# Kernel optimization log

Measured on AMD Instinct MI355X. Metric: run time of the kernel, lower is better.

Reference implementation:

```python
import jax, jax.numpy as jnp
import numpy as np

SEP = 64  # separate_number


def _get_histogram(M, sep):
    # torch code detaches + moves to CPU: no gradient flows through the histogram
    M = jax.lax.stop_gradient(M)
    mn = jnp.min(M)
    mx = jnp.max(M)
    interval = (mx - mn) / sep
    # equal-width binning; last bin is inclusive of max (clip handles it)
    idx = jnp.clip(jnp.floor((M - mn) / interval).astype(jnp.int32), 0, sep - 1)
    hist = jnp.zeros((sep,), dtype=M.dtype).at[idx.ravel()].add(1.0)
    return jax.nn.sigmoid(hist)


def setup_inputs() -> dict:
    key = jax.random.key(0)
    k1, k2, k3 = jax.random.split(key, 3)
    N, D = 8192, 256
    current_feature = jax.random.normal(k1, (N, D), dtype=jnp.float32)
    previous_feature = jax.random.normal(k2, (N, D), dtype=jnp.float32)
    # nn.Linear(separate_number, hidden_dim=1, bias=False) weight: [1, SEP]
    W = jax.random.normal(k3, (1, SEP), dtype=jnp.float32) * (1.0 / np.sqrt(SEP))
    return {"current_feature": current_feature, "previous_feature": previous_feature, "W": W}


def reference(current_feature, previous_feature, W):
    sep = W.shape[1]
    # [N, N] similarity matrix
    M = jnp.matmul(current_feature, previous_feature.T)
    hist_left = _get_histogram(M, sep)
    # result_matrix_right = prev @ cur.T = M.T; a transpose has an identical
    # value histogram, so reuse M (same math, avoids a second NxN matmul)
    hist_right = _get_histogram(M, sep)
    beta = (hist_left + hist_right) / 2.0
    beta = jnp.matmul(beta, W.T)  # Linear, no bias -> [hidden_dim]
    return jax.nn.sigmoid(beta)
```

## Files before the change

### kernel.cpp

```cpp
#include <hip/hip_runtime.h>

typedef __attribute__((ext_vector_type(8))) short short8v;
typedef __attribute__((ext_vector_type(4))) float f32x4;

#define N_ROWS 8192
#define KSPLIT 768
#define SEP 64
#define TDET 65.0f
#define TEXACT 73.0f
#define VTOL 5.5f
#define LIST_CAP 524288u

__device__ inline unsigned f2ord(float x){
  unsigned u = __float_as_uint(x);
  return (u & 0x80000000u) ? ~u : (u | 0x80000000u);
}
__device__ inline float ord2f(unsigned u){
  unsigned b = (u & 0x80000000u) ? (u & 0x7fffffffu) : ~u;
  return __uint_as_float(b);
}
__device__ inline unsigned short bf16rn(float x){
  unsigned b = __float_as_uint(x);
  unsigned r = (b + 0x7fffu + ((b >> 16) & 1u)) >> 16;
  return (unsigned short)r;
}
__device__ inline void gload16(const void* g, void* l){
  __builtin_amdgcn_global_load_lds((const __attribute__((address_space(1))) void*)g,
                                   (__attribute__((address_space(3))) void*)l, 16, 0, 0);
}
__device__ inline int bin_of(float v, float mnv, float interval){
  float r = (v - mnv) / interval;
  int b = (int)floorf(r);
  return b < 0 ? 0 : (b > 63 ? 63 : b);
}

__global__ void split_kernel(const float* __restrict__ cur, const float* __restrict__ prev,
                             unsigned short* __restrict__ cur2, unsigned short* __restrict__ prev2,
                             unsigned* __restrict__ ctl){
  if (blockIdx.x == 0){
    if (threadIdx.x == 0){
      ctl[0] = 0xFFFFFFFFu; ctl[1] = 0u; ctl[2] = 1u; ctl[3] = 0u; ctl[4] = 0u;
    }
    if (threadIdx.x < 64) ctl[5 + threadIdx.x] = 0u;
  }
  int g = blockIdx.x * blockDim.x + threadIdx.x;
  int isB = (g >= (N_ROWS * 256 / 4)) ? 1 : 0;
  int t = g - isB * (N_ROWS * 256 / 4);
  const float4 v = ((const float4*)(isB ? prev : cur))[t];
  int row = t >> 6;
  int col = (t & 63) << 2;
  float xs[4] = {v.x, v.y, v.z, v.w};
  unsigned short h[4], l[4];
  #pragma unroll
  for (int j = 0; j < 4; ++j){
    unsigned short hb = bf16rn(xs[j]);
    float hf = __uint_as_float(((unsigned)hb) << 16);
    h[j] = hb;
    l[j] = bf16rn(xs[j] - hf);
  }
  unsigned short* dst = isB ? prev2 : cur2;
  size_t base = (size_t)row * KSPLIT + col;
  uint2 hw, lw;
  hw.x = (unsigned)h[0] | ((unsigned)h[1] << 16); hw.y = (unsigned)h[2] | ((unsigned)h[3] << 16);
  lw.x = (unsigned)l[0] | ((unsigned)l[1] << 16); lw.y = (unsigned)l[2] | ((unsigned)l[3] << 16);
  *(uint2*)(dst + base) = hw;
  if (!isB){
    *(uint2*)(dst + base + 256) = lw;
    *(uint2*)(dst + base + 512) = hw;
  } else {
    *(uint2*)(dst + base + 256) = hw;
    *(uint2*)(dst + base + 512) = lw;
  }
}

__global__ __launch_bounds__(256) void gemm_det(const unsigned short* __restrict__ A2,
                                                const unsigned short* __restrict__ B2,
                                                unsigned* __restrict__ idxq,
                                                unsigned* __restrict__ lcnt){
  __shared__ unsigned short Ab[2][128 * 32];
  __shared__ unsigned short Bb[2][256 * 32];

  const int tid  = threadIdx.x;
  const int lane = tid & 63;
  const int wave = tid >> 6;
  const int swz = ((blockIdx.x & 7) << 8) | (blockIdx.x >> 3);
  const int bm = swz >> 5;
  const int bn = swz & 31;
  const int wr = wave >> 1, wc = wave & 1;

  const size_t aBase = (size_t)bm * 128 * KSPLIT;
  const size_t bBase = (size_t)bn * 256 * KSPLIT;
  const int rsel = lane & 15;
  const int ksel = (lane >> 4) * 8;

  f32x4 acc[4][8];
  #pragma unroll
  for (int m = 0; m < 4; ++m)
    #pragma unroll
    for (int n = 0; n < 8; ++n)
      acc[m][n] = (f32x4){0.f, 0.f, 0.f, 0.f};

  auto STAGE = [&](int ks, int b){
    const int k0 = ks * 32;
    #pragma unroll
    for (int r = 0; r < 2; ++r){
      int id = tid + r * 256;
      gload16(A2 + aBase + (size_t)(id >> 2) * KSPLIT + (id & 3) * 8 + k0, &Ab[b][id * 8]);
    }
    #pragma unroll
    for (int r = 0; r < 4; ++r){
      int id = tid + r * 256;
      gload16(B2 + bBase + (size_t)(id >> 2) * KSPLIT + (id & 3) * 8 + k0, &Bb[b][id * 8]);
    }
  };
  auto COMPUTE = [&](int b){
    short8v a[4];
    #pragma unroll
    for (int m = 0; m < 4; ++m)
      a[m] = *(const short8v*)(&Ab[b][(wr * 64 + m * 16 + rsel) * 32 + ksel]);
    #pragma unroll
    for (int n = 0; n < 8; ++n){
      short8v bv = *(const short8v*)(&Bb[b][(wc * 128 + n * 16 + rsel) * 32 + ksel]);
      #pragma unroll
      for (int m = 0; m < 4; ++m)
        acc[m][n] = __builtin_amdgcn_mfma_f32_16x16x32_bf16(a[m], bv, acc[m][n], 0, 0, 0);
    }
  };

  STAGE(0, 0);
  __syncthreads();
  for (int ks = 0; ks < 8; ++ks){
    if (ks < 7) STAGE(ks + 1, (ks + 1) & 1);
    COMPUTE(ks & 1);
    __syncthreads();
  }

  #pragma unroll
  for (int h2 = 0; h2 < 2; ++h2){
    unsigned long long mask = 0ull;
    #pragma unroll
    for (int m = 0; m < 4; ++m)
      #pragma unroll
      for (int nn = 0; nn < 4; ++nn)
        #pragma unroll
        for (int q = 0; q < 4; ++q)
          if (fabsf(acc[m][h2 * 4 + nn][q]) > TDET)
            mask |= (1ull << ((m * 4 + nn) * 4 + q));
    int cnt = __popcll(mask);
    int pre = cnt;
    #pragma unroll
    for (int off = 1; off < 64; off <<= 1){
      int t = __shfl_up(pre, off);
      if (lane >= off) pre += t;
    }
    int tot = __shfl(pre, 63);
    int base = 0;
    if (lane == 63 && tot > 0) base = (int)atomicAdd(lcnt, (unsigned)tot);
    base = __shfl(base, 63);
    if (mask){
      unsigned kk = (unsigned)(base + pre - cnt);
      #pragma unroll
      for (int m = 0; m < 4; ++m)
        #pragma unroll
        for (int nn = 0; nn < 4; ++nn)
          #pragma unroll
          for (int q = 0; q < 4; ++q){
            int b = (m * 4 + nn) * 4 + q;
            if ((mask >> b) & 1ull){
              int n = h2 * 4 + nn;
              float v = acc[m][n][q];
              int i = bm * 128 + wr * 64 + m * 16 + ((lane >> 4) << 2) + q;
              int j = bn * 256 + wc * 128 + n * 16 + (lane & 15);
              int e = (int)((v + 144.0f) * (1.0f / 4.5f));
              e = e < 0 ? 0 : (e > 63 ? 63 : e);
              if (kk < LIST_CAP)
                idxq[kk] = ((unsigned)e << 26) | ((unsigned)i << 13) | (unsigned)j;
              ++kk;
            }
          }
    }
  }
}

template<int EPI>
__global__ __launch_bounds__(256) void gemm_kernel(const unsigned short* __restrict__ A2,
                                                   const unsigned short* __restrict__ B2,
                                                   unsigned* __restrict__ mm,
                                                   unsigned* __restrict__ hist,
                                                   const unsigned* __restrict__ flag){
  if (flag[0] == 0u) return;
  __shared__ unsigned short As[128 * 32];
  __shared__ unsigned short Bs[128 * 32];

  const int tid  = threadIdx.x;
  const int lane = tid & 63;
  const int wave = tid >> 6;
  const int swz = ((blockIdx.x & 7) << 9) | (blockIdx.x >> 3);
  const int bm = swz >> 6;
  const int bn = swz & 63;
  const int wr = wave >> 1, wc = wave & 1;

  const size_t aBase = (size_t)bm * 128 * KSPLIT;
  const size_t bBase = (size_t)bn * 128 * KSPLIT;
  const int id0 = tid, id1 = tid + 256;
  const size_t aOff0 = aBase + (size_t)(id0 >> 2) * KSPLIT + (id0 & 3) * 8;
  const size_t aOff1 = aBase + (size_t)(id1 >> 2) * KSPLIT + (id1 & 3) * 8;
  const size_t bOff0 = bBase + (size_t)(id0 >> 2) * KSPLIT + (id0 & 3) * 8;
  const size_t bOff1 = bBase + (size_t)(id1 >> 2) * KSPLIT + (id1 & 3) * 8;

  f32x4 acc[4][4];
  #pragma unroll
  for (int m = 0; m < 4; ++m)
    #pragma unroll
    for (int n = 0; n < 4; ++n)
      acc[m][n] = (f32x4){0.f, 0.f, 0.f, 0.f};

  const int rsel = lane & 15;
  const int ksel = (lane >> 4) * 8;

  for (int ks = 0; ks < 24; ++ks){
    const int k0 = ks * 32;
    gload16(A2 + aOff0 + k0, As + id0 * 8);
    gload16(A2 + aOff1 + k0, As + id1 * 8);
    gload16(B2 + bOff0 + k0, Bs + id0 * 8);
    gload16(B2 + bOff1 + k0, Bs + id1 * 8);
    __syncthreads();
    short8v a[4], b[4];
    #pragma unroll
    for (int m = 0; m < 4; ++m)
      a[m] = *(const short8v*)(As + (wr * 64 + m * 16 + rsel) * 32 + ksel);
    #pragma unroll
    for (int n = 0; n < 4; ++n)
      b[n] = *(const short8v*)(Bs + (wc * 64 + n * 16 + rsel) * 32 + ksel);
    #pragma unroll
    for (int m = 0; m < 4; ++m)
      #pragma unroll
      for (int n = 0; n < 4; ++n)
        acc[m][n] = __builtin_amdgcn_mfma_f32_16x16x32_bf16(a[m], b[n], acc[m][n], 0, 0, 0);
    __syncthreads();
  }

  float*    red = (float*)As;
  unsigned* lh  = (unsigned*)((char*)As + 64);

  if (EPI == 0){
    float mn = 3.4e38f, mx = -3.4e38f;
    #pragma unroll
    for (int m = 0; m < 4; ++m)
      #pragma unroll
      for (int n = 0; n < 4; ++n)
        #pragma unroll
        for (int q = 0; q < 4; ++q){
          float v = acc[m][n][q];
          mn = fminf(mn, v); mx = fmaxf(mx, v);
        }
    #pragma unroll
    for (int off = 32; off; off >>= 1){
      mn = fminf(mn, __shfl_xor(mn, off));
      mx = fmaxf(mx, __shfl_xor(mx, off));
    }
    if (lane == 0){ red[wave] = mn; red[4 + wave] = mx; }
    __syncthreads();
    if (tid == 0){
      mn = fminf(fminf(red[0], red[1]), fminf(red[2], red[3]));
      mx = fmaxf(fmaxf(red[4], red[5]), fmaxf(red[6], red[7]));
      atomicMin(mm + 0, f2ord(mn));
      atomicMax(mm + 1, f2ord(mx));
    }
  }
  if (EPI == 2){
    if (tid < SEP) lh[tid] = 0u;
    __syncthreads();
    const float mnv = ord2f(mm[0]);
    const float mxv = ord2f(mm[1]);
    const float interval = (mxv - mnv) / 64.0f;
    #pragma unroll
    for (int m = 0; m < 4; ++m)
      #pragma unroll
      for (int n = 0; n < 4; ++n)
        #pragma unroll
        for (int q = 0; q < 4; ++q)
          atomicAdd(&lh[bin_of(acc[m][n][q], mnv, interval)], 1u);
    __syncthreads();
    if (tid < SEP){ unsigned c = lh[tid]; if (c) atomicAdd(hist + tid, c); }
  }
}

__global__ __launch_bounds__(256) void recompute_kernel(const float* __restrict__ cur,
                                                        const float* __restrict__ prev,
                                                        const unsigned* __restrict__ idxq,
                                                        const unsigned* __restrict__ lcnt,
                                                        unsigned* __restrict__ mm,
                                                        unsigned* __restrict__ viol,
                                                        float* __restrict__ vex){
  const int lane = threadIdx.x & 63;
  const int w  = (blockIdx.x * blockDim.x + threadIdx.x) >> 6;
  const int nw = (gridDim.x * blockDim.x) >> 6;
  unsigned n = lcnt[0]; if (n > LIST_CAP) n = LIST_CAP;
  float wmn = 3.4e38f, wmx = -3.4e38f;
  bool any = false;
  for (unsigned c = w; c < n; c += (unsigned)nw){
    unsigned u = idxq[c];
    int i = (int)((u >> 13) & 8191u), j = (int)(u & 8191u);
    float4 a = ((const float4*)cur)[i * 64 + lane];
    float4 b = ((const float4*)prev)[j * 64 + lane];
    float s = a.x * b.x + a.y * b.y + a.z * b.z + a.w * b.w;
    #pragma unroll
    for (int off = 32; off; off >>= 1) s += __shfl_xor(s, off);
    if (lane == 0){
      vex[c] = s;
      float dq = ((float)(u >> 26) + 0.5f) * 4.5f - 144.0f;
      if (fabsf(s - dq) > VTOL) atomicAdd(viol, 1u);
    }
    wmn = fminf(wmn, s); wmx = fmaxf(wmx, s);
    any = true;
  }
  if (lane == 0 && any){
    atomicMin(mm + 0, f2ord(wmn));
    atomicMax(mm + 1, f2ord(wmx));
  }
}

__global__ __launch_bounds__(256) void finalize2_kernel(const unsigned* __restrict__ mm,
                                                        const unsigned* __restrict__ lcnt,
                                                        const unsigned* __restrict__ viol,
                                                        const float* __restrict__ vex,
                                                        const float* __restrict__ W,
                                                        unsigned* __restrict__ flag,
                                                        float* __restrict__ out){
  __shared__ unsigned h[SEP];
  __shared__ unsigned okf;
  const int tid = threadIdx.x;
  if (tid < SEP) h[tid] = 0u;
  __syncthreads();
  const float mnv = ord2f(mm[0]);
  const float mxv = ord2f(mm[1]);
  const float interval = (mxv - mnv) / 64.0f;
  const unsigned cnt = lcnt[0];
  const unsigned n = cnt > LIST_CAP ? LIST_CAP : cnt;
  for (unsigned i = tid; i < n; i += 256u)
    atomicAdd(&h[bin_of(vex[i], mnv, interval)], 1u);
  __syncthreads();
  if (tid == 0){
    const int bLO = bin_of(-TEXACT, mnv, interval);
    const int bHI = bin_of( TEXACT, mnv, interval);
    bool ok = (cnt <= LIST_CAP) && (viol[0] == 0u) && (bLO >= 3) && (bHI <= 60) && (bLO < bHI)
              && (h[bLO - 1] >= 30u) && (h[bHI + 1] >= 30u);
    okf = ok ? 1u : 0u;
    if (ok) flag[0] = 0u;
    h[SEP - 1] = h[SEP - 1];
  }
  __syncthreads();
  if (!okf) return;
  if (tid < 64){
    const int bLO = bin_of(-TEXACT, mnv, interval);
    const int bHI = bin_of( TEXACT, mnv, interval);
    float beta;
    if (tid < bLO || tid > bHI) beta = 1.f / (1.f + expf(-(float)h[tid]));
    else beta = 1.0f;
    float p = beta * W[tid];
    #pragma unroll
    for (int off = 32; off; off >>= 1) p += __shfl_down(p, off);
    if (tid == 0) out[0] = 1.f / (1.f + expf(-p));
  }
}

__global__ void fin_kernel(const unsigned* __restrict__ hist, const float* __restrict__ W,
                           const unsigned* __restrict__ flag, float* __restrict__ out){
  if (flag[0] == 0u) return;
  int j = threadIdx.x;
  float beta = 1.f / (1.f + expf(-(float)hist[j]));
  float p = beta * W[j];
  #pragma unroll
  for (int off = 32; off; off >>= 1) p += __shfl_down(p, off);
  if (j == 0) out[0] = 1.f / (1.f + expf(-p));
}

extern "C" void kernel_launch(void* const* d_in, const int* in_sizes, int n_in,
                              void* d_out, int out_size, void* d_ws, size_t ws_size,
                              hipStream_t stream){
  const float* cur  = (const float*)d_in[0];
  const float* prev = (const float*)d_in[1];
  const float* W    = (const float*)d_in[2];
  float* out = (float*)d_out;
  char* ws = (char*)d_ws;

  unsigned short* cur2  = (unsigned short*)ws;
  unsigned short* prev2 = (unsigned short*)(ws + 12582912);
  unsigned* ctl   = (unsigned*)(ws + 25165824);
  unsigned* mm    = ctl + 0;
  unsigned* flag  = ctl + 2;
  unsigned* lcnt  = ctl + 3;
  unsigned* viol  = ctl + 4;
  unsigned* hist  = ctl + 5;
  unsigned* idxq  = (unsigned*)(ws + 25166592);
  float*    vex   = (float*)(ws + 27263744);
  const size_t NEED_NEW = 29360896;

  split_kernel<<<4096, 256, 0, stream>>>(cur, prev, cur2, prev2, ctl);

  if (ws_size >= NEED_NEW){
    gemm_det<<<2048, 256, 0, stream>>>(cur2, prev2, idxq, lcnt);
    recompute_kernel<<<256, 256, 0, stream>>>(cur, prev, idxq, lcnt, mm, viol, vex);
    finalize2_kernel<<<1, 256, 0, stream>>>(mm, lcnt, viol, vex, W, flag, out);
    gemm_kernel<0><<<4096, 256, 0, stream>>>(cur2, prev2, mm, hist, flag);
    gemm_kernel<2><<<4096, 256, 0, stream>>>(cur2, prev2, mm, hist, flag);
    fin_kernel<<<1, 64, 0, stream>>>(hist, W, flag, out);
  } else {
    gemm_kernel<0><<<4096, 256, 0, stream>>>(cur2, prev2, mm, hist, flag);
    gemm_kernel<2><<<4096, 256, 0, stream>>>(cur2, prev2, mm, hist, flag);
    fin_kernel<<<1, 64, 0, stream>>>(hist, W, flag, out);
  }
}
```

Baseline: 212.3 us.

## Fuse exact fp32 recompute of tail candidates into detection GEMM

The detection GEMM now uses 128x128 tiles (4096 blocks) instead of 128x256. Each block gathers its above-threshold candidates in LDS and recomputes their exact fp32 dot products in place, writing vex/idxq and updating the global min/max. This removes the separate recompute kernel launch and the global round trip of the candidate list. In exchange it adds per-block LDS staging with a cap of 2048 candidates, where overflow is flagged as a violation, plus a tail phase inside the GEMM that may leave the matrix units idle.

Result: slower. 226.0 us (+6.4%).

```diff
diff --git a/kernel.cpp b/kernel.cpp
--- a/kernel.cpp
+++ b/kernel.cpp
@@ -10,6 +10,7 @@
 #define TEXACT 73.0f
 #define VTOL 5.5f
 #define LIST_CAP 524288u
+#define CAND_CAP 2048u
 
 __device__ inline unsigned f2ord(float x){
   unsigned u = __float_as_uint(x);
@@ -75,56 +76,65 @@
 
 __global__ __launch_bounds__(256) void gemm_det(const unsigned short* __restrict__ A2,
                                                 const unsigned short* __restrict__ B2,
+                                                const float* __restrict__ cur,
+                                                const float* __restrict__ prev,
                                                 unsigned* __restrict__ idxq,
-                                                unsigned* __restrict__ lcnt){
+                                                float* __restrict__ vex,
+                                                unsigned* __restrict__ lcnt,
+                                                unsigned* __restrict__ mm,
+                                                unsigned* __restrict__ viol){
   __shared__ unsigned short Ab[2][128 * 32];
-  __shared__ unsigned short Bb[2][256 * 32];
+  __shared__ unsigned short Bb[2][128 * 32];
+  __shared__ unsigned bcnt, gbase, ccap;
 
   const int tid  = threadIdx.x;
   const int lane = tid & 63;
   const int wave = tid >> 6;
-  const int swz = ((blockIdx.x & 7) << 8) | (blockIdx.x >> 3);
-  const int bm = swz >> 5;
-  const int bn = swz & 31;
+  const int swz = ((blockIdx.x & 7) << 9) | (blockIdx.x >> 3);
+  const int bm = swz >> 6;
+  const int bn = swz & 63;
   const int wr = wave >> 1, wc = wave & 1;
 
+  if (tid == 0) bcnt = 0u;
+
   const size_t aBase = (size_t)bm * 128 * KSPLIT;
-  const size_t bBase = (size_t)bn * 256 * KSPLIT;
+  const size_t bBase = (size_t)bn * 128 * KSPLIT;
+  const int id0 = tid, id1 = tid + 256;
+  const size_t aOff0 = aBase + (size_t)(id0 >> 2) * KSPLIT + (id0 & 3) * 8;
+  const size_t aOff1 = aBase + (size_t)(id1 >> 2) * KSPLIT + (id1 & 3) * 8;
+  const size_t bOff0 = bBase + (size_t)(id0 >> 2) * KSPLIT + (id0 & 3) * 8;
+  const size_t bOff1 = bBase + (size_t)(id1 >> 2) * KSPLIT + (id1 & 3) * 8;
+
+  f32x4 acc[4][4];
+  #pragma unroll
+  for (int m = 0; m < 4; ++m)
+    #pragma unroll
+    for (int n = 0; n < 4; ++n)
+      acc[m][n] = (f32x4){0.f, 0.f, 0.f, 0.f};
+
   const int rsel = lane & 15;
   const int ksel = (lane >> 4) * 8;
 
-  f32x4 acc[4][8];
-  #pragma unroll
-  for (int m = 0; m < 4; ++m)
-    #pragma unroll
-    for (int n = 0; n < 8; ++n)
-      acc[m][n] = (f32x4){0.f, 0.f, 0.f, 0.f};
-
   auto STAGE = [&](int ks, int b){
     const int k0 = ks * 32;
-    #pragma unroll
-    for (int r = 0; r < 2; ++r){
-      int id = tid + r * 256;
-      gload16(A2 + aBase + (size_t)(id >> 2) * KSPLIT + (id & 3) * 8 + k0, &Ab[b][id * 8]);
-    }
-    #pragma unroll
-    for (int r = 0; r < 4; ++r){
-      int id = tid + r * 256;
-      gload16(B2 + bBase + (size_t)(id >> 2) * KSPLIT + (id & 3) * 8 + k0, &Bb[b][id * 8]);
-    }
+    gload16(A2 + aOff0 + k0, &Ab[b][id0 * 8]);
+    gload16(A2 + aOff1 + k0, &Ab[b][id1 * 8]);
+    gload16(B2 + bOff0 + k0, &Bb[b][id0 * 8]);
+    gload16(B2 + bOff1 + k0, &Bb[b][id1 * 8]);
   };
   auto COMPUTE = [&](int b){
-    short8v a[4];
+    short8v a[4], bv[4];
     #pragma unroll
     for (int m = 0; m < 4; ++m)
       a[m] = *(const short8v*)(&Ab[b][(wr * 64 + m * 16 + rsel) * 32 + ksel]);
     #pragma unroll
-    for (int n = 0; n < 8; ++n){
-      short8v bv = *(const short8v*)(&Bb[b][(wc * 128 + n * 16 + rsel) * 32 + ksel]);
-      #pragma unroll
-      for (int m = 0; m < 4; ++m)
-        acc[m][n] = __builtin_amdgcn_mfma_f32_16x16x32_bf16(a[m], bv, acc[m][n], 0, 0, 0);
-    }
+    for (int n = 0; n < 4; ++n)
+      bv[n] = *(const short8v*)(&Bb[b][(wc * 64 + n * 16 + rsel) * 32 + ksel]);
+    #pragma unroll
+    for (int m = 0; m < 4; ++m)
+      #pragma unroll
+      for (int n = 0; n < 4; ++n)
+        acc[m][n] = __builtin_amdgcn_mfma_f32_16x16x32_bf16(a[m], bv[n], acc[m][n], 0, 0, 0);
   };
 
   STAGE(0, 0);
@@ -135,50 +145,83 @@
     __syncthreads();
   }
 
-  #pragma unroll
-  for (int h2 = 0; h2 < 2; ++h2){
-    unsigned long long mask = 0ull;
-    #pragma unroll
-    for (int m = 0; m < 4; ++m)
-      #pragma unroll
-      for (int nn = 0; nn < 4; ++nn)
+  unsigned* cand = (unsigned*)Ab;
+
+  unsigned long long mask = 0ull;
+  #pragma unroll
+  for (int m = 0; m < 4; ++m)
+    #pragma unroll
+    for (int n = 0; n < 4; ++n)
+      #pragma unroll
+      for (int q = 0; q < 4; ++q)
+        if (fabsf(acc[m][n][q]) > TDET)
+          mask |= (1ull << ((m * 4 + n) * 4 + q));
+  int cnt = __popcll(mask);
+  int pre = cnt;
+  #pragma unroll
+  for (int off = 1; off < 64; off <<= 1){
+    int t = __shfl_up(pre, off);
+    if (lane >= off) pre += t;
+  }
+  int tot = __shfl(pre, 63);
+  unsigned wbase = 0;
+  if (lane == 63 && tot > 0) wbase = atomicAdd(&bcnt, (unsigned)tot);
+  wbase = __shfl((int)wbase, 63);
+  if (mask){
+    unsigned kk = wbase + (unsigned)(pre - cnt);
+    #pragma unroll
+    for (int m = 0; m < 4; ++m)
+      #pragma unroll
+      for (int n = 0; n < 4; ++n)
         #pragma unroll
-        for (int q = 0; q < 4; ++q)
-          if (fabsf(acc[m][h2 * 4 + nn][q]) > TDET)
-            mask |= (1ull << ((m * 4 + nn) * 4 + q));
-    int cnt = __popcll(mask);
-    int pre = cnt;
-    #pragma unroll
-    for (int off = 1; off < 64; off <<= 1){
-      int t = __shfl_up(pre, off);
-      if (lane >= off) pre += t;
+        for (int q = 0; q < 4; ++q){
+          int b = (m * 4 + n) * 4 + q;
+          if ((mask >> b) & 1ull){
+            float v = acc[m][n][q];
+            int i = bm * 128 + wr * 64 + m * 16 + ((lane >> 4) << 2) + q;
+            int j = bn * 128 + wc * 64 + n * 16 + (lane & 15);
+            int e = (int)((v + 144.0f) * (1.0f / 4.5f));
+            e = e < 0 ? 0 : (e > 63 ? 63 : e);
+            if (kk < CAND_CAP)
+              cand[kk] = ((unsigned)e << 26) | ((unsigned)i << 13) | (unsigned)j;
+            ++kk;
+          }
+        }
+  }
+  __syncthreads();
+  if (tid == 0){
+    unsigned c = bcnt;
+    unsigned cc = c > CAND_CAP ? CAND_CAP : c;
+    if (c > CAND_CAP) atomicAdd(viol, 1u);
+    gbase = cc ? atomicAdd(lcnt, cc) : 0u;
+    ccap = cc;
+  }
+  __syncthreads();
+
+  const unsigned cc = ccap, gb = gbase;
+  float wmn = 3.4e38f, wmx = -3.4e38f;
+  bool any = false;
+  for (unsigned c = (unsigned)wave; c < cc; c += 4u){
+    unsigned u = cand[c];
+    int i = (int)((u >> 13) & 8191u), j = (int)(u & 8191u);
+    float4 a = ((const float4*)cur)[i * 64 + lane];
+    float4 b = ((const float4*)prev)[j * 64 + lane];
+    float s = a.x * b.x + a.y * b.y + a.z * b.z + a.w * b.w;
+    #pragma unroll
+    for (int off = 32; off; off >>= 1) s += __shfl_xor(s, off);
+    unsigned gi = gb + c;
+    if (lane == 0 && gi < LIST_CAP){
+      vex[gi]  = s;
+      idxq[gi] = u;
+      float dq = ((float)(u >> 26) + 0.5f) * 4.5f - 144.0f;
+      if (fabsf(s - dq) > VTOL) atomicAdd(viol, 1u);
     }
-    int tot = __shfl(pre, 63);
-    int base = 0;
-    if (lane == 63 && tot > 0) base = (int)atomicAdd(lcnt, (unsigned)tot);
-    base = __shfl(base, 63);
-    if (mask){
-      unsigned kk = (unsigned)(base + pre - cnt);
-      #pragma unroll
-      for (int m = 0; m < 4; ++m)
-        #pragma unroll
-        for (int nn = 0; nn < 4; ++nn)
-          #pragma unroll
-          for (int q = 0; q < 4; ++q){
-            int b = (m * 4 + nn) * 4 + q;
-            if ((mask >> b) & 1ull){
-              int n = h2 * 4 + nn;
-              float v = acc[m][n][q];
-              int i = bm * 128 + wr * 64 + m * 16 + ((lane >> 4) << 2) + q;
-              int j = bn * 256 + wc * 128 + n * 16 + (lane & 15);
-              int e = (int)((v + 144.0f) * (1.0f / 4.5f));
-              e = e < 0 ? 0 : (e > 63 ? 63 : e);
-              if (kk < LIST_CAP)
-                idxq[kk] = ((unsigned)e << 26) | ((unsigned)i << 13) | (unsigned)j;
-              ++kk;
-            }
-          }
-    }
+    wmn = fminf(wmn, s); wmx = fmaxf(wmx, s);
+    any = true;
+  }
+  if (lane == 0 && any){
+    atomicMin(mm + 0, f2ord(wmn));
+    atomicMax(mm + 1, f2ord(wmx));
   }
 }
 
@@ -283,41 +326,6 @@
           atomicAdd(&lh[bin_of(acc[m][n][q], mnv, interval)], 1u);
     __syncthreads();
     if (tid < SEP){ unsigned c = lh[tid]; if (c) atomicAdd(hist + tid, c); }
-  }
-}
-
-__global__ __launch_bounds__(256) void recompute_kernel(const float* __restrict__ cur,
-                                                        const float* __restrict__ prev,
-                                                        const unsigned* __restrict__ idxq,
-                                                        const unsigned* __restrict__ lcnt,
-                                                        unsigned* __restrict__ mm,
-                                                        unsigned* __restrict__ viol,
-                                                        float* __restrict__ vex){
-  const int lane = threadIdx.x & 63;
-  const int w  = (blockIdx.x * blockDim.x + threadIdx.x) >> 6;
-  const int nw = (gridDim.x * blockDim.x) >> 6;
-  unsigned n = lcnt[0]; if (n > LIST_CAP) n = LIST_CAP;
-  float wmn = 3.4e38f, wmx = -3.4e38f;
-  bool any = false;
-  for (unsigned c = w; c < n; c += (unsigned)nw){
-    unsigned u = idxq[c];
-    int i = (int)((u >> 13) & 8191u), j = (int)(u & 8191u);
-    float4 a = ((const float4*)cur)[i * 64 + lane];
-    float4 b = ((const float4*)prev)[j * 64 + lane];
-    float s = a.x * b.x + a.y * b.y + a.z * b.z + a.w * b.w;
-    #pragma unroll
-    for (int off = 32; off; off >>= 1) s += __shfl_xor(s, off);
-    if (lane == 0){
-      vex[c] = s;
-      float dq = ((float)(u >> 26) + 0.5f) * 4.5f - 144.0f;
-      if (fabsf(s - dq) > VTOL) atomicAdd(viol, 1u);
-    }
-    wmn = fminf(wmn, s); wmx = fmaxf(wmx, s);
-    any = true;
-  }
-  if (lane == 0 && any){
-    atomicMin(mm + 0, f2ord(wmn));
-    atomicMax(mm + 1, f2ord(wmx));
   }
 }
 
@@ -348,7 +356,6 @@
               && (h[bLO - 1] >= 30u) && (h[bHI + 1] >= 30u);
     okf = ok ? 1u : 0u;
     if (ok) flag[0] = 0u;
-    h[SEP - 1] = h[SEP - 1];
   }
   __syncthreads();
   if (!okf) return;
@@ -400,8 +407,7 @@
   split_kernel<<<4096, 256, 0, stream>>>(cur, prev, cur2, prev2, ctl);
 
   if (ws_size >= NEED_NEW){
-    gemm_det<<<2048, 256, 0, stream>>>(cur2, prev2, idxq, lcnt);
-    recompute_kernel<<<256, 256, 0, stream>>>(cur, prev, idxq, lcnt, mm, viol, vex);
+    gemm_det<<<4096, 256, 0, stream>>>(cur2, prev2, cur, prev, idxq, vex, lcnt, mm, viol);
     finalize2_kernel<<<1, 256, 0, stream>>>(mm, lcnt, viol, vex, W, flag, out);
     gemm_kernel<0><<<4096, 256, 0, stream>>>(cur2, prev2, mm, hist, flag);
     gemm_kernel<2><<<4096, 256, 0, stream>>>(cur2, prev2, mm, hist, flag);
```
